# Kernel tuning notes

Measured on AMD Instinct MI355X. Metric: run time of the kernel, lower is better.

## Reference

```python
import jax, jax.numpy as jnp
import numpy as np

N, E, EQ, DIM = 50000, 800000, 100000, 256


def setup_inputs() -> dict:
    key = jax.random.key(0)
    k1, k2, k3, k4, k5 = jax.random.split(key, 5)
    edges = jax.random.randint(k1, (2, EQ), 0, N)
    adj_row = jax.random.randint(k2, (E,), 0, N)
    adj_col = jax.random.randint(k3, (E,), 0, N)
    node_weight = jax.random.uniform(k4, (N,), dtype=jnp.float32)
    # torchhd-style bipolar hypervectors scaled by sqrt(1/dim)
    scale = (1.0 / DIM) ** 0.5
    node_vectors = jnp.sign(jax.random.normal(k5, (N, DIM), dtype=jnp.float32)) * scale
    return dict(edges=edges, adj_row=adj_row, adj_col=adj_col,
                node_weight=node_weight, node_vectors=node_vectors)


def reference(edges, adj_row, adj_col, node_weight, node_vectors):
    n = node_vectors.shape[0]
    # get_random_node_vectors: embedding * node_weight
    x = node_vectors * node_weight[:, None]                       # [N, dim]
    # one_hop_x = A @ x ; two_hop_x = A @ one_hop_x (binary adjacency)
    one_hop = jax.ops.segment_sum(x[adj_col], adj_row, num_segments=n)       # [N, dim]
    two_hop = jax.ops.segment_sum(one_hop[adj_col], adj_row, num_segments=n)  # [N, dim]
    deg = jax.ops.segment_sum(jnp.ones(adj_row.shape, x.dtype), adj_row, num_segments=n)  # [N]
    s, t = edges[0], edges[1]
    dot = lambda a, b: (a * b).sum(-1)
    count_1_1 = dot(one_hop[s], one_hop[t])
    count_1_2 = dot(one_hop[s], two_hop[t]) + dot(two_hop[s], one_hop[t])
    count_2_2 = dot(two_hop[s] - deg[s][:, None] * x[s],
                    two_hop[t] - deg[t][:, None] * x[t])
    count_self_1_2 = dot(one_hop[s], two_hop[s]) + dot(one_hop[t], two_hop[t])
    return (count_1_1, count_1_2, count_2_2, count_self_1_2)
```

## Files before the change

### kernel.cpp

```cpp
#include <hip/hip_runtime.h>

#define DIM 256
#define NODE_U2 192
#define NODE_U4 96
#define SLOT_OH_U2 64
#define SLOT_TH_U2 128
#define SLOT_OH_U4 32
#define SLOT_TH_U4 64

__device__ __forceinline__ unsigned int f2bf_rne(float f) {
    unsigned int u = __float_as_uint(f);
    return (u + 0x7fffu + ((u >> 16) & 1u)) >> 16;
}
__device__ __forceinline__ float bf_lo(unsigned int u) {
    return __uint_as_float(u << 16);
}
__device__ __forceinline__ float bf_hi(unsigned int u) {
    return __uint_as_float(u & 0xffff0000u);
}
__device__ __forceinline__ unsigned int pack2(float a, float b) {
    return f2bf_rne(a) | (f2bf_rne(b) << 16);
}

#define ACC8(v)                                            \
    do {                                                   \
        a0 += bf_lo((v).x); a1 += bf_hi((v).x);            \
        a2 += bf_lo((v).y); a3 += bf_hi((v).y);            \
        a4 += bf_lo((v).z); a5 += bf_hi((v).z);            \
        a6 += bf_lo((v).w); a7 += bf_hi((v).w);            \
    } while (0)

__global__ void compute_x_kernel(const float* __restrict__ nv,
                                 const float* __restrict__ w,
                                 uint2* __restrict__ cmb,
                                 int total_u2) {
    int i = blockIdx.x * blockDim.x + threadIdx.x;
    int stride = gridDim.x * blockDim.x;
    for (; i < total_u2; i += stride) {
        float4 v = reinterpret_cast<const float4*>(nv)[i];
        int node = i >> 6;
        int j = i & 63;
        float wt = w[node];
        uint2 r;
        r.x = pack2(v.x * wt, v.y * wt);
        r.y = pack2(v.z * wt, v.w * wt);
        cmb[(size_t)node * NODE_U2 + j] = r;
    }
}

__global__ void hist_kernel(const int* __restrict__ row,
                            int* __restrict__ cnt, int nedges) {
    int e = blockIdx.x * blockDim.x + threadIdx.x;
    if (e < nedges) atomicAdd(&cnt[row[e]], 1);
}

__global__ void block_sum_kernel(const int* __restrict__ cnt,
                                 int* __restrict__ sums, int n) {
    __shared__ int lds[256];
    int i = blockIdx.x * 256 + threadIdx.x;
    lds[threadIdx.x] = (i < n) ? cnt[i] : 0;
    __syncthreads();
    #pragma unroll
    for (int off = 128; off > 0; off >>= 1) {
        if (threadIdx.x < off) lds[threadIdx.x] += lds[threadIdx.x + off];
        __syncthreads();
    }
    if (threadIdx.x == 0) sums[blockIdx.x] = lds[0];
}

__global__ void scan_sums_kernel(int* __restrict__ sums, int nb,
                                 int* __restrict__ row_ptr_n) {
    __shared__ int lds[256];
    int v = (threadIdx.x < nb) ? sums[threadIdx.x] : 0;
    lds[threadIdx.x] = v;
    __syncthreads();
    #pragma unroll
    for (int off = 1; off < 256; off <<= 1) {
        int t = (threadIdx.x >= off) ? lds[threadIdx.x - off] : 0;
        __syncthreads();
        lds[threadIdx.x] += t;
        __syncthreads();
    }
    if (threadIdx.x < nb) sums[threadIdx.x] = lds[threadIdx.x] - v;
    if (threadIdx.x == 255) *row_ptr_n = lds[255];
}

__global__ void scan_block_kernel(const int* __restrict__ cnt,
                                  const int* __restrict__ sums,
                                  int* __restrict__ row_ptr,
                                  int* __restrict__ cursor, int n) {
    __shared__ int lds[256];
    int i = blockIdx.x * 256 + threadIdx.x;
    int v = (i < n) ? cnt[i] : 0;
    lds[threadIdx.x] = v;
    __syncthreads();
    #pragma unroll
    for (int off = 1; off < 256; off <<= 1) {
        int t = (threadIdx.x >= off) ? lds[threadIdx.x - off] : 0;
        __syncthreads();
        lds[threadIdx.x] += t;
        __syncthreads();
    }
    if (i < n) {
        int excl = sums[blockIdx.x] + lds[threadIdx.x] - v;
        row_ptr[i] = excl;
        cursor[i] = excl;
    }
}

__global__ void scatter_perm_kernel(const int* __restrict__ row,
                                    const int* __restrict__ col,
                                    int* __restrict__ cursor,
                                    int* __restrict__ perm, int nedges) {
    int e = blockIdx.x * blockDim.x + threadIdx.x;
    if (e < nedges) {
        int pos = atomicAdd(&cursor[row[e]], 1);
        perm[pos] = col[e];
    }
}

__global__ void gather_hop_kernel(const int* __restrict__ row_ptr,
                                  const int* __restrict__ perm,
                                  const uint4* __restrict__ src,
                                  uint4* __restrict__ dst, int n) {
    int gid = blockIdx.x * blockDim.x + threadIdx.x;
    int r = gid >> 6;
    if (r >= n) return;
    int lane = gid & 63;
    int h = lane >> 5;
    int l = lane & 31;

    int beg = row_ptr[r];
    int end = row_ptr[r + 1];

    float a0 = 0.f, a1 = 0.f, a2 = 0.f, a3 = 0.f;
    float a4 = 0.f, a5 = 0.f, a6 = 0.f, a7 = 0.f;

    int e = beg + h;
    while (e + 6 < end) {
        int c0 = perm[e];
        int c1 = perm[e + 2];
        int c2 = perm[e + 4];
        int c3 = perm[e + 6];
        uint4 v0 = src[(size_t)c0 * NODE_U4 + l];
        uint4 v1 = src[(size_t)c1 * NODE_U4 + l];
        uint4 v2 = src[(size_t)c2 * NODE_U4 + l];
        uint4 v3 = src[(size_t)c3 * NODE_U4 + l];
        ACC8(v0); ACC8(v1); ACC8(v2); ACC8(v3);
        e += 8;
    }
    while (e < end) {
        int c0 = perm[e];
        uint4 v0 = src[(size_t)c0 * NODE_U4 + l];
        ACC8(v0);
        e += 2;
    }

    a0 += __shfl_xor(a0, 32); a1 += __shfl_xor(a1, 32);
    a2 += __shfl_xor(a2, 32); a3 += __shfl_xor(a3, 32);
    a4 += __shfl_xor(a4, 32); a5 += __shfl_xor(a5, 32);
    a6 += __shfl_xor(a6, 32); a7 += __shfl_xor(a7, 32);

    if (lane < 32) {
        uint4 o;
        o.x = pack2(a0, a1);
        o.y = pack2(a2, a3);
        o.z = pack2(a4, a5);
        o.w = pack2(a6, a7);
        dst[(size_t)r * NODE_U4 + l] = o;
    }
}

__global__ void query_kernel(const int* __restrict__ es,
                             const int* __restrict__ et,
                             const uint4* __restrict__ cmb4,
                             const int* __restrict__ row_ptr,
                             float* __restrict__ out, int nq) {
    int gid = blockIdx.x * blockDim.x + threadIdx.x;
    int q = gid >> 5;
    if (q >= nq) return;
    int l = gid & 31;

    int s = es[q];
    int t = et[q];

    const uint4* ns = cmb4 + (size_t)s * NODE_U4;
    const uint4* nt = cmb4 + (size_t)t * NODE_U4;

    uint4 vxs = ns[l];
    uint4 vos = ns[SLOT_OH_U4 + l];
    uint4 vts = ns[SLOT_TH_U4 + l];
    uint4 vxt = nt[l];
    uint4 vot = nt[SLOT_OH_U4 + l];
    uint4 vtt = nt[SLOT_TH_U4 + l];
    float ds = (float)(row_ptr[s + 1] - row_ptr[s]);
    float dt = (float)(row_ptr[t + 1] - row_ptr[t]);

    float c11 = 0.f, c12 = 0.f, c22 = 0.f, cs = 0.f;
    const unsigned int* pxs = (const unsigned int*)&vxs;
    const unsigned int* pxt = (const unsigned int*)&vxt;
    const unsigned int* pos_ = (const unsigned int*)&vos;
    const unsigned int* pot = (const unsigned int*)&vot;
    const unsigned int* pts = (const unsigned int*)&vts;
    const unsigned int* ptt = (const unsigned int*)&vtt;
    #pragma unroll
    for (int k = 0; k < 4; ++k) {
        {
            float fxs = bf_lo(pxs[k]), fxt = bf_lo(pxt[k]);
            float fos = bf_lo(pos_[k]), fot = bf_lo(pot[k]);
            float fts = bf_lo(pts[k]), ftt = bf_lo(ptt[k]);
            c11 += fos * fot;
            c12 += fos * ftt + fts * fot;
            float as = fts - ds * fxs;
            float bt = ftt - dt * fxt;
            c22 += as * bt;
            cs  += fos * fts + fot * ftt;
        }
        {
            float fxs = bf_hi(pxs[k]), fxt = bf_hi(pxt[k]);
            float fos = bf_hi(pos_[k]), fot = bf_hi(pot[k]);
            float fts = bf_hi(pts[k]), ftt = bf_hi(ptt[k]);
            c11 += fos * fot;
            c12 += fos * ftt + fts * fot;
            float as = fts - ds * fxs;
            float bt = ftt - dt * fxt;
            c22 += as * bt;
            cs  += fos * fts + fot * ftt;
        }
    }

    #pragma unroll
    for (int off = 16; off > 0; off >>= 1) {
        c11 += __shfl_xor(c11, off);
        c12 += __shfl_xor(c12, off);
        c22 += __shfl_xor(c22, off);
        cs  += __shfl_xor(cs,  off);
    }

    if (l == 0) {
        out[q]          = c11;
        out[nq + q]     = c12;
        out[2 * nq + q] = c22;
        out[3 * nq + q] = cs;
    }
}

extern "C" void kernel_launch(void* const* d_in, const int* in_sizes, int n_in,
                              void* d_out, int out_size, void* d_ws, size_t ws_size,
                              hipStream_t stream) {
    const int*   edges        = (const int*)  d_in[0];
    const int*   adj_row      = (const int*)  d_in[1];
    const int*   adj_col      = (const int*)  d_in[2];
    const float* node_weight  = (const float*)d_in[3];
    const float* node_vectors = (const float*)d_in[4];

    const int EQ = in_sizes[0] / 2;
    const int E  = in_sizes[1];
    const int N  = in_sizes[3];

    uint2* cmb = (uint2*)d_ws;
    int* row_ptr = (int*)(cmb + (size_t)N * NODE_U2);
    int* cursor  = row_ptr + (N + 1);
    int* cnt     = cursor + N;
    int* perm    = cnt + N;
    int* sums    = perm + E;

    const int* es = edges;
    const int* et = edges + EQ;
    float* out = (float*)d_out;

    int nb = (N + 255) / 256;

    hipMemsetAsync(cnt, 0, (size_t)N * sizeof(int), stream);
    hist_kernel<<<(E + 255) / 256, 256, 0, stream>>>(adj_row, cnt, E);
    block_sum_kernel<<<nb, 256, 0, stream>>>(cnt, sums, N);
    scan_sums_kernel<<<1, 256, 0, stream>>>(sums, nb, row_ptr + N);
    scan_block_kernel<<<nb, 256, 0, stream>>>(cnt, sums, row_ptr, cursor, N);
    scatter_perm_kernel<<<(E + 255) / 256, 256, 0, stream>>>(adj_row, adj_col,
                                                             cursor, perm, E);

    int total_u2 = N * 64;
    compute_x_kernel<<<2048, 256, 0, stream>>>(node_vectors, node_weight, cmb,
                                               total_u2);

    const uint4* cmb4 = (const uint4*)cmb;
    int gthreads = N * 64;
    int gblocks = (gthreads + 255) / 256;
    gather_hop_kernel<<<gblocks, 256, 0, stream>>>(
        row_ptr, perm, cmb4, (uint4*)cmb4 + SLOT_OH_U4, N);
    gather_hop_kernel<<<gblocks, 256, 0, stream>>>(
        row_ptr, perm, cmb4 + SLOT_OH_U4, (uint4*)cmb4 + SLOT_TH_U4, N);

    int qthreads = EQ * 32;
    query_kernel<<<(qthreads + 255) / 256, 256, 0, stream>>>(
        es, et, cmb4, row_ptr, out, EQ);
}
```

Before: 270.9 us.

## Batch gather loads with inline asm and fuse histogram into x kernel

The gather kernel now issues eight index loads, then eight 16-byte row loads back to back using inline global_load asm with explicit vmcnt waits, so more memory requests are in flight per wave. The remainder is handled in chunks of 8 and 4 edges, then singles. Separately, the degree histogram is folded into the x-scaling kernel, which removes one launch. Explicit waitcnt and sched barriers limit compiler scheduling and raise register use, which may lower occupancy.

```diff
diff --git a/kernel.cpp b/kernel.cpp
--- a/kernel.cpp
+++ b/kernel.cpp
@@ -8,6 +8,8 @@
 #define SLOT_OH_U4 32
 #define SLOT_TH_U4 64
 
+typedef unsigned int u32x4 __attribute__((ext_vector_type(4)));
+
 __device__ __forceinline__ unsigned int f2bf_rne(float f) {
     unsigned int u = __float_as_uint(f);
     return (u + 0x7fffu + ((u >> 16) & 1u)) >> 16;
@@ -22,21 +24,33 @@
     return f2bf_rne(a) | (f2bf_rne(b) << 16);
 }
 
-#define ACC8(v)                                            \
-    do {                                                   \
-        a0 += bf_lo((v).x); a1 += bf_hi((v).x);            \
-        a2 += bf_lo((v).y); a3 += bf_hi((v).y);            \
-        a4 += bf_lo((v).z); a5 += bf_hi((v).z);            \
-        a6 += bf_lo((v).w); a7 += bf_hi((v).w);            \
+#define GLD_U4(dstv, p) \
+    asm volatile("global_load_dwordx4 %0, %1, off" : "=v"(dstv) : "v"(p))
+#define GLD_DW(dsts, p) \
+    asm volatile("global_load_dword %0, %1, off" : "=v"(dsts) : "v"(p))
+#define VMWAIT(n)                                                        \
+    do {                                                                 \
+        asm volatile("s_waitcnt vmcnt(%0)" ::"i"(n) : "memory");         \
+        __builtin_amdgcn_sched_barrier(0);                               \
     } while (0)
 
-__global__ void compute_x_kernel(const float* __restrict__ nv,
-                                 const float* __restrict__ w,
-                                 uint2* __restrict__ cmb,
-                                 int total_u2) {
-    int i = blockIdx.x * blockDim.x + threadIdx.x;
+#define ACC8V(v)                                          \
+    do {                                                  \
+        a0 += bf_lo((v)[0]); a1 += bf_hi((v)[0]);         \
+        a2 += bf_lo((v)[1]); a3 += bf_hi((v)[1]);         \
+        a4 += bf_lo((v)[2]); a5 += bf_hi((v)[2]);         \
+        a6 += bf_lo((v)[3]); a7 += bf_hi((v)[3]);         \
+    } while (0)
+
+__global__ void x_and_hist_kernel(const float* __restrict__ nv,
+                                  const float* __restrict__ w,
+                                  uint2* __restrict__ cmb,
+                                  int total_u2,
+                                  const int* __restrict__ adj_row,
+                                  int* __restrict__ cnt, int E) {
+    int i0 = blockIdx.x * blockDim.x + threadIdx.x;
     int stride = gridDim.x * blockDim.x;
-    for (; i < total_u2; i += stride) {
+    for (int i = i0; i < total_u2; i += stride) {
         float4 v = reinterpret_cast<const float4*>(nv)[i];
         int node = i >> 6;
         int j = i & 63;
@@ -46,12 +60,9 @@
         r.y = pack2(v.z * wt, v.w * wt);
         cmb[(size_t)node * NODE_U2 + j] = r;
     }
-}
-
-__global__ void hist_kernel(const int* __restrict__ row,
-                            int* __restrict__ cnt, int nedges) {
-    int e = blockIdx.x * blockDim.x + threadIdx.x;
-    if (e < nedges) atomicAdd(&cnt[row[e]], 1);
+    for (int e = i0; e < E; e += stride) {
+        atomicAdd(&cnt[adj_row[e]], 1);
+    }
 }
 
 __global__ void block_sum_kernel(const int* __restrict__ cnt,
@@ -121,8 +132,8 @@
 
 __global__ void gather_hop_kernel(const int* __restrict__ row_ptr,
                                   const int* __restrict__ perm,
-                                  const uint4* __restrict__ src,
-                                  uint4* __restrict__ dst, int n) {
+                                  const u32x4* __restrict__ src,
+                                  u32x4* __restrict__ dst, int n) {
     int gid = blockIdx.x * blockDim.x + threadIdx.x;
     int r = gid >> 6;
     if (r >= n) return;
@@ -132,28 +143,67 @@
 
     int beg = row_ptr[r];
     int end = row_ptr[r + 1];
+    int len = end - beg;
+    int nb8 = len >> 4;
+    int rem = len & 15;
 
     float a0 = 0.f, a1 = 0.f, a2 = 0.f, a3 = 0.f;
     float a4 = 0.f, a5 = 0.f, a6 = 0.f, a7 = 0.f;
 
-    int e = beg + h;
-    while (e + 6 < end) {
-        int c0 = perm[e];
-        int c1 = perm[e + 2];
-        int c2 = perm[e + 4];
-        int c3 = perm[e + 6];
-        uint4 v0 = src[(size_t)c0 * NODE_U4 + l];
-        uint4 v1 = src[(size_t)c1 * NODE_U4 + l];
-        uint4 v2 = src[(size_t)c2 * NODE_U4 + l];
-        uint4 v3 = src[(size_t)c3 * NODE_U4 + l];
-        ACC8(v0); ACC8(v1); ACC8(v2); ACC8(v3);
-        e += 8;
-    }
-    while (e < end) {
-        int c0 = perm[e];
-        uint4 v0 = src[(size_t)c0 * NODE_U4 + l];
-        ACC8(v0);
-        e += 2;
+    for (int b = 0; b < nb8; ++b) {
+        const int* pp = perm + beg + (b << 4) + (h << 3);
+        int c0, c1, c2, c3, c4, c5, c6, c7;
+        GLD_DW(c0, pp + 0); GLD_DW(c1, pp + 1);
+        GLD_DW(c2, pp + 2); GLD_DW(c3, pp + 3);
+        GLD_DW(c4, pp + 4); GLD_DW(c5, pp + 5);
+        GLD_DW(c6, pp + 6); GLD_DW(c7, pp + 7);
+        VMWAIT(0);
+        u32x4 v0, v1, v2, v3, v4, v5, v6, v7;
+        GLD_U4(v0, src + (size_t)(unsigned)c0 * NODE_U4 + l);
+        GLD_U4(v1, src + (size_t)(unsigned)c1 * NODE_U4 + l);
+        GLD_U4(v2, src + (size_t)(unsigned)c2 * NODE_U4 + l);
+        GLD_U4(v3, src + (size_t)(unsigned)c3 * NODE_U4 + l);
+        GLD_U4(v4, src + (size_t)(unsigned)c4 * NODE_U4 + l);
+        GLD_U4(v5, src + (size_t)(unsigned)c5 * NODE_U4 + l);
+        GLD_U4(v6, src + (size_t)(unsigned)c6 * NODE_U4 + l);
+        GLD_U4(v7, src + (size_t)(unsigned)c7 * NODE_U4 + l);
+        VMWAIT(4);
+        ACC8V(v0); ACC8V(v1); ACC8V(v2); ACC8V(v3);
+        VMWAIT(0);
+        ACC8V(v4); ACC8V(v5); ACC8V(v6); ACC8V(v7);
+    }
+
+    int tb = beg + (nb8 << 4);
+    if (rem & 8) {
+        const int* pp = perm + tb + (h << 2);
+        int c0, c1, c2, c3;
+        GLD_DW(c0, pp + 0); GLD_DW(c1, pp + 1);
+        GLD_DW(c2, pp + 2); GLD_DW(c3, pp + 3);
+        VMWAIT(0);
+        u32x4 v0, v1, v2, v3;
+        GLD_U4(v0, src + (size_t)(unsigned)c0 * NODE_U4 + l);
+        GLD_U4(v1, src + (size_t)(unsigned)c1 * NODE_U4 + l);
+        GLD_U4(v2, src + (size_t)(unsigned)c2 * NODE_U4 + l);
+        GLD_U4(v3, src + (size_t)(unsigned)c3 * NODE_U4 + l);
+        VMWAIT(0);
+        ACC8V(v0); ACC8V(v1); ACC8V(v2); ACC8V(v3);
+        tb += 8;
+    }
+    if (rem & 4) {
+        const int* pp = perm + tb + (h << 1);
+        int c0, c1;
+        GLD_DW(c0, pp + 0); GLD_DW(c1, pp + 1);
+        VMWAIT(0);
+        u32x4 v0, v1;
+        GLD_U4(v0, src + (size_t)(unsigned)c0 * NODE_U4 + l);
+        GLD_U4(v1, src + (size_t)(unsigned)c1 * NODE_U4 + l);
+        VMWAIT(0);
+        ACC8V(v0); ACC8V(v1);
+        tb += 4;
+    }
+    for (int e = tb + h; e < end; e += 2) {
+        u32x4 v = src[(size_t)(unsigned)perm[e] * NODE_U4 + l];
+        ACC8V(v);
     }
 
     a0 += __shfl_xor(a0, 32); a1 += __shfl_xor(a1, 32);
@@ -162,11 +212,11 @@
     a6 += __shfl_xor(a6, 32); a7 += __shfl_xor(a7, 32);
 
     if (lane < 32) {
-        uint4 o;
-        o.x = pack2(a0, a1);
-        o.y = pack2(a2, a3);
-        o.z = pack2(a4, a5);
-        o.w = pack2(a6, a7);
+        u32x4 o;
+        o[0] = pack2(a0, a1);
+        o[1] = pack2(a2, a3);
+        o[2] = pack2(a4, a5);
+        o[3] = pack2(a6, a7);
         dst[(size_t)r * NODE_U4 + l] = o;
     }
 }
@@ -272,26 +322,25 @@
     int nb = (N + 255) / 256;
 
     hipMemsetAsync(cnt, 0, (size_t)N * sizeof(int), stream);
-    hist_kernel<<<(E + 255) / 256, 256, 0, stream>>>(adj_row, cnt, E);
+    int total_u2 = N * 64;
+    x_and_hist_kernel<<<2048, 256, 0, stream>>>(node_vectors, node_weight, cmb,
+                                                total_u2, adj_row, cnt, E);
+
     block_sum_kernel<<<nb, 256, 0, stream>>>(cnt, sums, N);
     scan_sums_kernel<<<1, 256, 0, stream>>>(sums, nb, row_ptr + N);
     scan_block_kernel<<<nb, 256, 0, stream>>>(cnt, sums, row_ptr, cursor, N);
     scatter_perm_kernel<<<(E + 255) / 256, 256, 0, stream>>>(adj_row, adj_col,
                                                              cursor, perm, E);
 
-    int total_u2 = N * 64;
-    compute_x_kernel<<<2048, 256, 0, stream>>>(node_vectors, node_weight, cmb,
-                                               total_u2);
-
-    const uint4* cmb4 = (const uint4*)cmb;
+    const u32x4* cmb4 = (const u32x4*)cmb;
     int gthreads = N * 64;
     int gblocks = (gthreads + 255) / 256;
     gather_hop_kernel<<<gblocks, 256, 0, stream>>>(
-        row_ptr, perm, cmb4, (uint4*)cmb4 + SLOT_OH_U4, N);
+        row_ptr, perm, cmb4, (u32x4*)cmb4 + SLOT_OH_U4, N);
     gather_hop_kernel<<<gblocks, 256, 0, stream>>>(
-        row_ptr, perm, cmb4 + SLOT_OH_U4, (uint4*)cmb4 + SLOT_TH_U4, N);
+        row_ptr, perm, cmb4 + SLOT_OH_U4, (u32x4*)cmb4 + SLOT_TH_U4, N);
 
     int qthreads = EQ * 32;
     query_kernel<<<(qthreads + 255) / 256, 256, 0, stream>>>(
-        es, et, cmb4, row_ptr, out, EQ);
-}
+        es, et, (const uint4*)cmb4, row_ptr, out, EQ);
+}
```

After: 270.6 us. No clear change (-0.1%).

## Bucket CSR neighbors by column range and fuse histogram into x kernel

Applied to the files above, without the earlier changes.

Builds the CSR with a composite key of row and column bucket (16 buckets of 4096 columns), so each row's neighbor list comes out partially sorted by column. Gathers in the hop kernels then touch nearby source rows, which should improve cache locality. The edge histogram is folded into the x-scaling kernel to save a launch. The cost is a counter array 16 times larger and a two-level scan over N*16 entries, plus an extra row-pointer extraction kernel.

```diff
diff --git a/kernel.cpp b/kernel.cpp
--- a/kernel.cpp
+++ b/kernel.cpp
@@ -8,6 +8,9 @@
 #define SLOT_OH_U4 32
 #define SLOT_TH_U4 64
 
+#define CB_SHIFT 12
+#define CB 16
+
 __device__ __forceinline__ unsigned int f2bf_rne(float f) {
     unsigned int u = __float_as_uint(f);
     return (u + 0x7fffu + ((u >> 16) & 1u)) >> 16;
@@ -30,13 +33,16 @@
         a6 += bf_lo((v).w); a7 += bf_hi((v).w);            \
     } while (0)
 
-__global__ void compute_x_kernel(const float* __restrict__ nv,
-                                 const float* __restrict__ w,
-                                 uint2* __restrict__ cmb,
-                                 int total_u2) {
-    int i = blockIdx.x * blockDim.x + threadIdx.x;
+__global__ void x_and_hist_kernel(const float* __restrict__ nv,
+                                  const float* __restrict__ w,
+                                  uint2* __restrict__ cmb,
+                                  int total_u2,
+                                  const int* __restrict__ adj_row,
+                                  const int* __restrict__ adj_col,
+                                  int* __restrict__ cnt2, int E) {
+    int i0 = blockIdx.x * blockDim.x + threadIdx.x;
     int stride = gridDim.x * blockDim.x;
-    for (; i < total_u2; i += stride) {
+    for (int i = i0; i < total_u2; i += stride) {
         float4 v = reinterpret_cast<const float4*>(nv)[i];
         int node = i >> 6;
         int j = i & 63;
@@ -46,19 +52,17 @@
         r.y = pack2(v.z * wt, v.w * wt);
         cmb[(size_t)node * NODE_U2 + j] = r;
     }
-}
-
-__global__ void hist_kernel(const int* __restrict__ row,
-                            int* __restrict__ cnt, int nedges) {
-    int e = blockIdx.x * blockDim.x + threadIdx.x;
-    if (e < nedges) atomicAdd(&cnt[row[e]], 1);
-}
-
-__global__ void block_sum_kernel(const int* __restrict__ cnt,
+    for (int e = i0; e < E; e += stride) {
+        int key = adj_row[e] * CB + (adj_col[e] >> CB_SHIFT);
+        atomicAdd(&cnt2[key], 1);
+    }
+}
+
+__global__ void block_sum_kernel(const int* __restrict__ in,
                                  int* __restrict__ sums, int n) {
     __shared__ int lds[256];
     int i = blockIdx.x * 256 + threadIdx.x;
-    lds[threadIdx.x] = (i < n) ? cnt[i] : 0;
+    lds[threadIdx.x] = (i < n) ? in[i] : 0;
     __syncthreads();
     #pragma unroll
     for (int off = 128; off > 0; off >>= 1) {
@@ -69,7 +73,7 @@
 }
 
 __global__ void scan_sums_kernel(int* __restrict__ sums, int nb,
-                                 int* __restrict__ row_ptr_n) {
+                                 int* __restrict__ total_out) {
     __shared__ int lds[256];
     int v = (threadIdx.x < nb) ? sums[threadIdx.x] : 0;
     lds[threadIdx.x] = v;
@@ -82,16 +86,16 @@
         __syncthreads();
     }
     if (threadIdx.x < nb) sums[threadIdx.x] = lds[threadIdx.x] - v;
-    if (threadIdx.x == 255) *row_ptr_n = lds[255];
-}
-
-__global__ void scan_block_kernel(const int* __restrict__ cnt,
+    if (threadIdx.x == 255) *total_out = lds[255];
+}
+
+__global__ void scan_block_kernel(const int* __restrict__ in,
                                   const int* __restrict__ sums,
-                                  int* __restrict__ row_ptr,
-                                  int* __restrict__ cursor, int n) {
+                                  int* __restrict__ out1,
+                                  int* __restrict__ out2, int n) {
     __shared__ int lds[256];
     int i = blockIdx.x * 256 + threadIdx.x;
-    int v = (i < n) ? cnt[i] : 0;
+    int v = (i < n) ? in[i] : 0;
     lds[threadIdx.x] = v;
     __syncthreads();
     #pragma unroll
@@ -103,19 +107,27 @@
     }
     if (i < n) {
         int excl = sums[blockIdx.x] + lds[threadIdx.x] - v;
-        row_ptr[i] = excl;
-        cursor[i] = excl;
-    }
+        out1[i] = excl;
+        out2[i] = excl;
+    }
+}
+
+__global__ void extract_rowptr_kernel(const int* __restrict__ cur2,
+                                      int* __restrict__ row_ptr, int n) {
+    int i = blockIdx.x * blockDim.x + threadIdx.x;
+    if (i < n) row_ptr[i] = cur2[(size_t)i * CB];
 }
 
 __global__ void scatter_perm_kernel(const int* __restrict__ row,
                                     const int* __restrict__ col,
-                                    int* __restrict__ cursor,
+                                    int* __restrict__ cursor2,
                                     int* __restrict__ perm, int nedges) {
     int e = blockIdx.x * blockDim.x + threadIdx.x;
     if (e < nedges) {
-        int pos = atomicAdd(&cursor[row[e]], 1);
-        perm[pos] = col[e];
+        int c = col[e];
+        int key = row[e] * CB + (c >> CB_SHIFT);
+        int pos = atomicAdd(&cursor2[key], 1);
+        perm[pos] = c;
     }
 }
 
@@ -260,28 +272,36 @@
 
     uint2* cmb = (uint2*)d_ws;
     int* row_ptr = (int*)(cmb + (size_t)N * NODE_U2);
-    int* cursor  = row_ptr + (N + 1);
-    int* cnt     = cursor + N;
-    int* perm    = cnt + N;
-    int* sums    = perm + E;
+    int* cnt2    = row_ptr + (N + 1);
+    int* cur2    = cnt2 + (size_t)N * CB;
+    int* cursor2 = cur2 + (size_t)N * CB;
+    int* perm    = cursor2 + (size_t)N * CB;
+    int* s1      = perm + E;
+    int* s2      = s1 + ((size_t)N * CB + 255) / 256 + 8;
 
     const int* es = edges;
     const int* et = edges + EQ;
     float* out = (float*)d_out;
 
-    int nb = (N + 255) / 256;
-
-    hipMemsetAsync(cnt, 0, (size_t)N * sizeof(int), stream);
-    hist_kernel<<<(E + 255) / 256, 256, 0, stream>>>(adj_row, cnt, E);
-    block_sum_kernel<<<nb, 256, 0, stream>>>(cnt, sums, N);
-    scan_sums_kernel<<<1, 256, 0, stream>>>(sums, nb, row_ptr + N);
-    scan_block_kernel<<<nb, 256, 0, stream>>>(cnt, sums, row_ptr, cursor, N);
+    const int n0  = N * CB;
+    const int nb0 = (n0 + 255) / 256;
+    const int nb1 = (nb0 + 255) / 256;
+
+    hipMemsetAsync(cnt2, 0, (size_t)n0 * sizeof(int), stream);
+    int total_u2 = N * 64;
+    x_and_hist_kernel<<<2048, 256, 0, stream>>>(node_vectors, node_weight, cmb,
+                                                total_u2, adj_row, adj_col,
+                                                cnt2, E);
+
+    block_sum_kernel<<<nb0, 256, 0, stream>>>(cnt2, s1, n0);
+    block_sum_kernel<<<nb1, 256, 0, stream>>>(s1, s2, nb0);
+    scan_sums_kernel<<<1, 256, 0, stream>>>(s2, nb1, row_ptr + N);
+    scan_block_kernel<<<nb1, 256, 0, stream>>>(s1, s2, s1, s1, nb0);
+    scan_block_kernel<<<nb0, 256, 0, stream>>>(cnt2, s1, cur2, cursor2, n0);
+    extract_rowptr_kernel<<<(N + 255) / 256, 256, 0, stream>>>(cur2, row_ptr, N);
+
     scatter_perm_kernel<<<(E + 255) / 256, 256, 0, stream>>>(adj_row, adj_col,
-                                                             cursor, perm, E);
-
-    int total_u2 = N * 64;
-    compute_x_kernel<<<2048, 256, 0, stream>>>(node_vectors, node_weight, cmb,
-                                               total_u2);
+                                                             cursor2, perm, E);
 
     const uint4* cmb4 = (const uint4*)cmb;
     int gthreads = N * 64;
```

Result: slower. 276.6 us (+2.1%).

## Slice feature dim into 8 column slabs for cache-friendly SpMM gathers

Applied to the files above, without the earlier changes.

Stores x and one-hop vectors in a column-sliced layout (8 slices of 32 dims per node) and assigns each block to one slice for 64 rows, so the gathered working set per slice (~3.2 MB) can stay in L2 and be reused across rows. Each row is handled by 4 threads that walk all edges sequentially, which removes the half-wave split and the cross-lane shuffle. The histogram is also folded into the x-compute kernel, saving one launch. The cost is extra writes for the sliced copies and more workspace, and each thread now makes less memory-level parallel progress per edge.

```diff
diff --git a/kernel.cpp b/kernel.cpp
--- a/kernel.cpp
+++ b/kernel.cpp
@@ -8,6 +8,8 @@
 #define SLOT_OH_U4 32
 #define SLOT_TH_U4 64
 
+#define NSL 8
+
 __device__ __forceinline__ unsigned int f2bf_rne(float f) {
     unsigned int u = __float_as_uint(f);
     return (u + 0x7fffu + ((u >> 16) & 1u)) >> 16;
@@ -30,13 +32,16 @@
         a6 += bf_lo((v).w); a7 += bf_hi((v).w);            \
     } while (0)
 
-__global__ void compute_x_kernel(const float* __restrict__ nv,
-                                 const float* __restrict__ w,
-                                 uint2* __restrict__ cmb,
-                                 int total_u2) {
-    int i = blockIdx.x * blockDim.x + threadIdx.x;
+__global__ void x_and_hist_kernel(const float* __restrict__ nv,
+                                  const float* __restrict__ w,
+                                  uint2* __restrict__ cmb,
+                                  uint2* __restrict__ xs_sl,
+                                  int total_u2, int N,
+                                  const int* __restrict__ adj_row,
+                                  int* __restrict__ cnt, int E) {
+    int i0 = blockIdx.x * blockDim.x + threadIdx.x;
     int stride = gridDim.x * blockDim.x;
-    for (; i < total_u2; i += stride) {
+    for (int i = i0; i < total_u2; i += stride) {
         float4 v = reinterpret_cast<const float4*>(nv)[i];
         int node = i >> 6;
         int j = i & 63;
@@ -45,20 +50,19 @@
         r.x = pack2(v.x * wt, v.y * wt);
         r.y = pack2(v.z * wt, v.w * wt);
         cmb[(size_t)node * NODE_U2 + j] = r;
-    }
-}
-
-__global__ void hist_kernel(const int* __restrict__ row,
-                            int* __restrict__ cnt, int nedges) {
-    int e = blockIdx.x * blockDim.x + threadIdx.x;
-    if (e < nedges) atomicAdd(&cnt[row[e]], 1);
-}
-
-__global__ void block_sum_kernel(const int* __restrict__ cnt,
+        int s = j >> 3;
+        xs_sl[((size_t)s * N + node) * 8 + (j & 7)] = r;
+    }
+    for (int e = i0; e < E; e += stride) {
+        atomicAdd(&cnt[adj_row[e]], 1);
+    }
+}
+
+__global__ void block_sum_kernel(const int* __restrict__ in,
                                  int* __restrict__ sums, int n) {
     __shared__ int lds[256];
     int i = blockIdx.x * 256 + threadIdx.x;
-    lds[threadIdx.x] = (i < n) ? cnt[i] : 0;
+    lds[threadIdx.x] = (i < n) ? in[i] : 0;
     __syncthreads();
     #pragma unroll
     for (int off = 128; off > 0; off >>= 1) {
@@ -69,7 +73,7 @@
 }
 
 __global__ void scan_sums_kernel(int* __restrict__ sums, int nb,
-                                 int* __restrict__ row_ptr_n) {
+                                 int* __restrict__ total_out) {
     __shared__ int lds[256];
     int v = (threadIdx.x < nb) ? sums[threadIdx.x] : 0;
     lds[threadIdx.x] = v;
@@ -82,16 +86,16 @@
         __syncthreads();
     }
     if (threadIdx.x < nb) sums[threadIdx.x] = lds[threadIdx.x] - v;
-    if (threadIdx.x == 255) *row_ptr_n = lds[255];
-}
-
-__global__ void scan_block_kernel(const int* __restrict__ cnt,
+    if (threadIdx.x == 255) *total_out = lds[255];
+}
+
+__global__ void scan_block_kernel(const int* __restrict__ in,
                                   const int* __restrict__ sums,
-                                  int* __restrict__ row_ptr,
-                                  int* __restrict__ cursor, int n) {
+                                  int* __restrict__ out1,
+                                  int* __restrict__ out2, int n) {
     __shared__ int lds[256];
     int i = blockIdx.x * 256 + threadIdx.x;
-    int v = (i < n) ? cnt[i] : 0;
+    int v = (i < n) ? in[i] : 0;
     lds[threadIdx.x] = v;
     __syncthreads();
     #pragma unroll
@@ -103,8 +107,8 @@
     }
     if (i < n) {
         int excl = sums[blockIdx.x] + lds[threadIdx.x] - v;
-        row_ptr[i] = excl;
-        cursor[i] = excl;
+        out1[i] = excl;
+        out2[i] = excl;
     }
 }
 
@@ -119,56 +123,52 @@
     }
 }
 
-__global__ void gather_hop_kernel(const int* __restrict__ row_ptr,
-                                  const int* __restrict__ perm,
-                                  const uint4* __restrict__ src,
-                                  uint4* __restrict__ dst, int n) {
-    int gid = blockIdx.x * blockDim.x + threadIdx.x;
-    int r = gid >> 6;
-    if (r >= n) return;
-    int lane = gid & 63;
-    int h = lane >> 5;
-    int l = lane & 31;
+__global__ void gather_sliced_kernel(const int* __restrict__ row_ptr,
+                                     const int* __restrict__ perm,
+                                     const uint4* __restrict__ src_sl,
+                                     uint4* __restrict__ dst_sl,
+                                     uint4* __restrict__ dst_cmb_slot,
+                                     int N) {
+    int s = blockIdx.x & (NSL - 1);
+    int rb = blockIdx.x >> 3;
+    int g = threadIdx.x >> 2;
+    int j = threadIdx.x & 3;
+    int r = rb * 64 + g;
+    if (r >= N) return;
 
     int beg = row_ptr[r];
     int end = row_ptr[r + 1];
 
+    const uint4* base = src_sl + (size_t)s * N * 4;
+
     float a0 = 0.f, a1 = 0.f, a2 = 0.f, a3 = 0.f;
     float a4 = 0.f, a5 = 0.f, a6 = 0.f, a7 = 0.f;
 
-    int e = beg + h;
-    while (e + 6 < end) {
+    int e = beg;
+    for (; e + 3 < end; e += 4) {
         int c0 = perm[e];
-        int c1 = perm[e + 2];
-        int c2 = perm[e + 4];
-        int c3 = perm[e + 6];
-        uint4 v0 = src[(size_t)c0 * NODE_U4 + l];
-        uint4 v1 = src[(size_t)c1 * NODE_U4 + l];
-        uint4 v2 = src[(size_t)c2 * NODE_U4 + l];
-        uint4 v3 = src[(size_t)c3 * NODE_U4 + l];
+        int c1 = perm[e + 1];
+        int c2 = perm[e + 2];
+        int c3 = perm[e + 3];
+        uint4 v0 = base[(size_t)c0 * 4 + j];
+        uint4 v1 = base[(size_t)c1 * 4 + j];
+        uint4 v2 = base[(size_t)c2 * 4 + j];
+        uint4 v3 = base[(size_t)c3 * 4 + j];
         ACC8(v0); ACC8(v1); ACC8(v2); ACC8(v3);
-        e += 8;
-    }
-    while (e < end) {
-        int c0 = perm[e];
-        uint4 v0 = src[(size_t)c0 * NODE_U4 + l];
-        ACC8(v0);
-        e += 2;
-    }
-
-    a0 += __shfl_xor(a0, 32); a1 += __shfl_xor(a1, 32);
-    a2 += __shfl_xor(a2, 32); a3 += __shfl_xor(a3, 32);
-    a4 += __shfl_xor(a4, 32); a5 += __shfl_xor(a5, 32);
-    a6 += __shfl_xor(a6, 32); a7 += __shfl_xor(a7, 32);
-
-    if (lane < 32) {
-        uint4 o;
-        o.x = pack2(a0, a1);
-        o.y = pack2(a2, a3);
-        o.z = pack2(a4, a5);
-        o.w = pack2(a6, a7);
-        dst[(size_t)r * NODE_U4 + l] = o;
-    }
+    }
+    for (; e < end; ++e) {
+        int c = perm[e];
+        uint4 v = base[(size_t)c * 4 + j];
+        ACC8(v);
+    }
+
+    uint4 o;
+    o.x = pack2(a0, a1);
+    o.y = pack2(a2, a3);
+    o.z = pack2(a4, a5);
+    o.w = pack2(a6, a7);
+    if (dst_sl) dst_sl[((size_t)s * N + r) * 4 + j] = o;
+    dst_cmb_slot[(size_t)r * NODE_U4 + s * 4 + j] = o;
 }
 
 __global__ void query_kernel(const int* __restrict__ es,
@@ -258,38 +258,43 @@
     const int E  = in_sizes[1];
     const int N  = in_sizes[3];
 
-    uint2* cmb = (uint2*)d_ws;
-    int* row_ptr = (int*)(cmb + (size_t)N * NODE_U2);
+    uint2* cmb   = (uint2*)d_ws;
+    uint2* xs_sl = cmb + (size_t)N * NODE_U2;
+    uint2* oh_sl = xs_sl + (size_t)N * NSL * 8;
+    int* row_ptr = (int*)(oh_sl + (size_t)N * NSL * 8);
     int* cursor  = row_ptr + (N + 1);
     int* cnt     = cursor + N;
     int* perm    = cnt + N;
-    int* sums    = perm + E;
+    int* s1      = perm + E;
 
     const int* es = edges;
     const int* et = edges + EQ;
     float* out = (float*)d_out;
 
-    int nb = (N + 255) / 256;
+    const int nb0 = (N + 255) / 256;
 
     hipMemsetAsync(cnt, 0, (size_t)N * sizeof(int), stream);
-    hist_kernel<<<(E + 255) / 256, 256, 0, stream>>>(adj_row, cnt, E);
-    block_sum_kernel<<<nb, 256, 0, stream>>>(cnt, sums, N);
-    scan_sums_kernel<<<1, 256, 0, stream>>>(sums, nb, row_ptr + N);
-    scan_block_kernel<<<nb, 256, 0, stream>>>(cnt, sums, row_ptr, cursor, N);
+    int total_u2 = N * 64;
+    x_and_hist_kernel<<<2048, 256, 0, stream>>>(node_vectors, node_weight,
+                                                cmb, xs_sl, total_u2, N,
+                                                adj_row, cnt, E);
+
+    block_sum_kernel<<<nb0, 256, 0, stream>>>(cnt, s1, N);
+    scan_sums_kernel<<<1, 256, 0, stream>>>(s1, nb0, row_ptr + N);
+    scan_block_kernel<<<nb0, 256, 0, stream>>>(cnt, s1, row_ptr, cursor, N);
     scatter_perm_kernel<<<(E + 255) / 256, 256, 0, stream>>>(adj_row, adj_col,
                                                              cursor, perm, E);
 
-    int total_u2 = N * 64;
-    compute_x_kernel<<<2048, 256, 0, stream>>>(node_vectors, node_weight, cmb,
-                                               total_u2);
-
-    const uint4* cmb4 = (const uint4*)cmb;
-    int gthreads = N * 64;
-    int gblocks = (gthreads + 255) / 256;
-    gather_hop_kernel<<<gblocks, 256, 0, stream>>>(
-        row_ptr, perm, cmb4, (uint4*)cmb4 + SLOT_OH_U4, N);
-    gather_hop_kernel<<<gblocks, 256, 0, stream>>>(
-        row_ptr, perm, cmb4 + SLOT_OH_U4, (uint4*)cmb4 + SLOT_TH_U4, N);
+    const uint4* xs4 = (const uint4*)xs_sl;
+    uint4* oh4 = (uint4*)oh_sl;
+    uint4* cmb4 = (uint4*)cmb;
+    int nrb = (N + 63) / 64;
+    int gblocks = nrb * NSL;
+    gather_sliced_kernel<<<gblocks, 256, 0, stream>>>(
+        row_ptr, perm, xs4, oh4, cmb4 + SLOT_OH_U4, N);
+    gather_sliced_kernel<<<gblocks, 256, 0, stream>>>(
+        row_ptr, perm, (const uint4*)oh4, (uint4*)nullptr,
+        cmb4 + SLOT_TH_U4, N);
 
     int qthreads = EQ * 32;
     query_kernel<<<(qthreads + 255) / 256, 256, 0, stream>>>(
```

Result: faster. 256.4 us (-5.4%).
